# Optimization experiments

Measured on AMD Instinct MI355X. Metric: run time of the kernel, lower is better.

## Reference

```python
import jax, jax.numpy as jnp
import numpy as np
import math

MUL = 128
N_NODES = 10000
N_EDGES = 131072
AVG_NEIGH = 16.0
# (l1 of node irrep, l2 of edge SH, output l3); sorted by output irrep like e3nn Irreps.sort
INSTR = [(0, 0, 0), (1, 1, 0), (0, 1, 1), (1, 0, 1), (1, 2, 1), (0, 2, 2), (1, 1, 2), (1, 3, 2), (0, 3, 3), (1, 2, 3)]
SH_OFF = [0, 1, 4, 9]  # offsets of l-blocks inside edge_attrs (dim 16 = 1+3+5+7)


def _su2_cg(j1, j2, j3):
    f = math.factorial
    C = np.zeros((2 * j1 + 1, 2 * j2 + 1, 2 * j3 + 1))
    for m1 in range(-j1, j1 + 1):
        for m2 in range(-j2, j2 + 1):
            m3 = m1 + m2
            if abs(m3) > j3:
                continue
            pref = (2 * j3 + 1) * f(j3 + j1 - j2) * f(j3 - j1 + j2) * f(j1 + j2 - j3) / f(j1 + j2 + j3 + 1)
            pref *= f(j3 + m3) * f(j3 - m3) * f(j1 - m1) * f(j1 + m1) * f(j2 - m2) * f(j2 + m2)
            s = 0.0
            for k in range(max(0, -(j3 - j2 + m1), -(j3 - j1 - m2)), min(j1 + j2 - j3, j1 - m1, j2 + m2) + 1):
                s += (-1.0) ** k / (f(k) * f(j1 + j2 - j3 - k) * f(j1 - m1 - k) * f(j2 + m2 - k) * f(j3 - j2 + m1 + k) * f(j3 - j1 - m2 + k))
            C[m1 + j1, m2 + j2, m3 + j3] = math.sqrt(pref) * s
    return C


def _q(l):
    # change of basis real->complex spherical harmonics (e3nn convention incl. (-i)^l phase)
    q = np.zeros((2 * l + 1, 2 * l + 1), dtype=np.complex128)
    for m in range(-l, 0):
        q[l + m, l + abs(m)] = 1 / math.sqrt(2)
        q[l + m, l - abs(m)] = -1j / math.sqrt(2)
    q[l, l] = 1.0
    for m in range(1, l + 1):
        q[l + m, l + abs(m)] = (-1) ** m / math.sqrt(2)
        q[l + m, l - abs(m)] = 1j * (-1) ** m / math.sqrt(2)
    return ((-1j) ** l) * q


def _w3j(l1, l2, l3):
    C = _su2_cg(l1, l2, l3).astype(np.complex128)
    Q1, Q2, Q3 = _q(l1), _q(l2), _q(l3)
    for q3 in (np.conj(Q3), Q3):
        D = np.einsum('abc,ai,bj,ck->ijk', C, Q1, Q2, q3)
        if np.abs(D.imag).max() < 1e-9:
            Dr = D.real
            return (Dr / np.linalg.norm(Dr)).astype(np.float32)
    raise ValueError('real wigner-3j construction failed')


W3J = {ins: _w3j(ins[0], ins[1], ins[2]) for ins in set(INSTR)}


def setup_inputs():
    ks = jax.random.split(jax.random.key(0), 15)
    return {
        'node_feats': jax.random.normal(ks[0], (N_NODES, 4 * MUL), jnp.float32),
        'node_attrs': jax.random.normal(ks[1], (N_NODES, 10), jnp.float32),
        'edge_attrs': jax.random.normal(ks[2], (N_EDGES, 16), jnp.float32),
        'edge_feats': jax.random.normal(ks[3], (N_EDGES, 8), jnp.float32),
        'edge_index': jax.random.randint(ks[4], (2, N_EDGES), 0, N_NODES, jnp.int32),
        'W_node_0': jax.random.normal(ks[5], (MUL, MUL), jnp.float32),
        'W_node_1': jax.random.normal(ks[6], (MUL, MUL), jnp.float32),
        'R_W0': jax.random.normal(ks[7], (8, 64), jnp.float32),
        'R_W1': jax.random.normal(ks[8], (64, 64), jnp.float32),
        'R_W2': jax.random.normal(ks[9], (64, 64), jnp.float32),
        'R_W3': jax.random.normal(ks[10], (64, len(INSTR) * MUL), jnp.float32),
        'W_out_0': jax.random.normal(ks[11], (2 * MUL, MUL), jnp.float32),
        'W_out_1': jax.random.normal(ks[12], (3 * MUL, MUL), jnp.float32),
        'W_out_2': jax.random.normal(ks[13], (3 * MUL, MUL), jnp.float32),
        'W_out_3': jax.random.normal(ks[14], (2 * MUL, MUL), jnp.float32),
    }


def reference(node_feats, node_attrs, edge_attrs, edge_feats, edge_index, W_node_0, W_node_1, R_W0, R_W1, R_W2, R_W3, W_out_0, W_out_1, W_out_2, W_out_3):
    sender, receiver = edge_index[0], edge_index[1]
    n = node_feats.shape[0]
    # self-interaction Linear (e3nn: per-irrep matmul, weight / sqrt(fan_in))
    h0 = jnp.einsum('nui,uv->nvi', node_feats[:, :MUL].reshape(n, MUL, 1), W_node_0) / math.sqrt(MUL)
    h1 = jnp.einsum('nui,uv->nvi', node_feats[:, MUL:].reshape(n, MUL, 3), W_node_1) / math.sqrt(MUL)
    # radial MLP [8,64,64,64,1280] with SiLU on hidden layers
    r = edge_feats
    for W in (R_W0, R_W1, R_W2):
        r = jax.nn.silu(r @ (W / math.sqrt(W.shape[0])))
    r = r @ (R_W3 / math.sqrt(R_W3.shape[0]))
    hs = (h0[sender], h1[sender])  # gather sender feats, [E, MUL, 2l1+1]
    outs = {0: [], 1: [], 2: [], 3: []}
    for k, (l1, l2, l3) in enumerate(INSTR):
        w3j = jnp.asarray(W3J[(l1, l2, l3)])
        sh = edge_attrs[:, SH_OFF[l2]:SH_OFF[l2] + 2 * l2 + 1]
        w = r[:, k * MUL:(k + 1) * MUL]
        hw = hs[l1] * w[:, :, None]                                    # radial-weighted sender feats
        c = jnp.einsum('ijk,ej->eik', w3j, sh)                         # [E, 2l1+1, 2l3+1]
        t = jnp.einsum('eik,eui->euk', c, hw) * math.sqrt(2 * l3 + 1)  # 'uvu' path, component-norm path weight
        outs[l3].append(jax.ops.segment_sum(t, receiver, num_segments=n))
    Wout = (W_out_0, W_out_1, W_out_2, W_out_3)
    blocks = []
    for l in range(4):
        cat = jnp.concatenate(outs[l], axis=1)  # simplify(): concat multiplicities per l
        blocks.append(jnp.einsum('nui,uv->nvi', cat, Wout[l]) / (math.sqrt(cat.shape[1]) * AVG_NEIGH))
    return jnp.concatenate(blocks, axis=-1)  # reshape_irreps -> [N, MUL, 16]
```

## Files before the change

kernel.cpp:

```cpp
#include <hip/hip_runtime.h>
#include <math.h>

#define NNODES 10000
#define NEDGES 131072
#define CHUNK 16

#define W3J_OFF 0
#define H_OFF   1280
#define R2_OFF  (1280 + NNODES*512)
#define CSR_W   (R2_OFF + NEDGES*64)
#define CNT_W   CSR_W
#define CUR_W   (CSR_W + NNODES)
#define OFF_W   (CSR_W + 2*NNODES)
#define ELIST_W (CSR_W + 2*NNODES + NNODES + 1)

constexpr int cL1[10]  = {0,1,0,1,1,0,1,1,0,1};
constexpr int cL2[10]  = {0,1,1,0,2,2,1,3,3,2};
constexpr int cN3[10]  = {1,1,3,3,3,5,5,5,7,7};
constexpr int cSHO[10] = {0,1,1,0,4,4,1,9,9,4};
constexpr int cCCO[11] = {0,1,4,7,16,25,30,45,60,67,88};
constexpr int cCATO[10]= {0,128,256,640,1024,1408,2048,2688,3328,4224};

struct cpx { double re, im; };
__device__ inline cpx cmul(cpx a, cpx b){ return {a.re*b.re - a.im*b.im, a.re*b.im + a.im*b.re}; }

__device__ double dfact(int n){ double r = 1.0; for (int i = 2; i <= n; ++i) r *= (double)i; return r; }

__device__ double cgval(int j1,int j2,int j3,int m1,int m2){
  int m3 = m1 + m2;
  if (m3 > j3 || m3 < -j3) return 0.0;
  double pref = (double)(2*j3+1) * dfact(j3+j1-j2)*dfact(j3-j1+j2)*dfact(j1+j2-j3)/dfact(j1+j2+j3+1);
  pref *= dfact(j3+m3)*dfact(j3-m3)*dfact(j1-m1)*dfact(j1+m1)*dfact(j2-m2)*dfact(j2+m2);
  int k0 = 0; if (-(j3-j2+m1) > k0) k0 = -(j3-j2+m1); if (-(j3-j1-m2) > k0) k0 = -(j3-j1-m2);
  int k1 = j1+j2-j3; if (j1-m1 < k1) k1 = j1-m1; if (j2+m2 < k1) k1 = j2+m2;
  double s = 0.0;
  for (int k = k0; k <= k1; ++k){
    double d = dfact(k)*dfact(j1+j2-j3-k)*dfact(j1-m1-k)*dfact(j2+m2-k)*dfact(j3-j2+m1+k)*dfact(j3-j1-m2+k);
    s += ((k & 1) ? -1.0 : 1.0) / d;
  }
  return sqrt(pref) * s;
}

__device__ cpx qval(int l, int a, int col){
  int m = a - l;
  const double is2 = 0.70710678118654752440;
  double re = 0.0, im = 0.0;
  if (m < 0){
    if (col == l - m) re = is2;
    else if (col == l + m) im = -is2;
  } else if (m == 0){
    if (col == l) re = 1.0;
  } else {
    double sgn = (m & 1) ? -1.0 : 1.0;
    if (col == l + m) re = sgn * is2;
    else if (col == l - m) im = sgn * is2;
  }
  double pr, pi;
  switch (l & 3){ case 0: pr=1; pi=0; break; case 1: pr=0; pi=-1; break; case 2: pr=-1; pi=0; break; default: pr=0; pi=1; }
  return { re*pr - im*pi, re*pi + im*pr };
}

__global__ void w3j_kernel(float* ws){
  __shared__ double red[128];
  __shared__ int useConjS;
  __shared__ double normS;
  const int IL[10][3] = {{0,0,0},{1,1,0},{0,1,1},{1,0,1},{1,2,1},{0,2,2},{1,1,2},{1,3,2},{0,3,3},{1,2,3}};
  int k = blockIdx.x;
  int l1 = IL[k][0], l2 = IL[k][1], l3 = IL[k][2];
  int n1 = 2*l1+1, n2 = 2*l2+1, n3 = 2*l3+1;
  int nent = n1*n2*n3;
  int tid = threadIdx.x;
  double dcr=0, dci=0, dpr=0, dpi=0;
  if (tid < nent){
    int i = tid/(n2*n3), j = (tid/n3)%n2, kk = tid%n3;
    for (int a = 0; a < n1; ++a){
      for (int b = 0; b < n2; ++b){
        int m1 = a - l1, m2 = b - l2, m3 = m1 + m2;
        if (m3 < -l3 || m3 > l3) continue;
        int c = m3 + l3;
        double C = cgval(l1,l2,l3,m1,m2);
        if (C == 0.0) continue;
        cpx q1 = qval(l1,a,i), q2 = qval(l2,b,j), q3 = qval(l3,c,kk);
        cpx t = cmul(q1,q2);
        cpx q3c = { q3.re, -q3.im };
        cpx tc = cmul(t, q3c);
        cpx tp = cmul(t, q3);
        dcr += C*tc.re; dci += C*tc.im;
        dpr += C*tp.re; dpi += C*tp.im;
      }
    }
  }
  red[tid] = (tid < nent) ? fabs(dci) : 0.0;
  __syncthreads();
  if (tid == 0){
    double mx = 0.0;
    for (int t = 0; t < 128; ++t) if (red[t] > mx) mx = red[t];
    useConjS = (mx < 1e-9) ? 1 : 0;
  }
  __syncthreads();
  double re = useConjS ? dcr : dpr;
  red[tid] = (tid < nent) ? re*re : 0.0;
  __syncthreads();
  if (tid == 0){
    double s = 0.0;
    for (int t = 0; t < 128; ++t) s += red[t];
    normS = sqrt(s);
  }
  __syncthreads();
  if (tid < nent)
    ws[W3J_OFF + k*128 + tid] = (float)(re / normS * sqrt((double)(2*l3+1)));
}

__launch_bounds__(256, 4)
__global__ void node_kernel(const float* __restrict__ nf, const float* __restrict__ W0,
                            const float* __restrict__ W1, float* __restrict__ ws){
  __shared__ float AtL[128*68];
  float* h = ws + H_OFF;
  int tid = threadIdx.x;
  int n0 = blockIdx.x * 64;
  const float rs = 0.08838834764831845f;
  int mg = (tid & 15) * 4;
  int vg = (tid >> 4) * 8;
  for (int c = 0; c < 4; ++c){
    __syncthreads();
    for (int idx = tid; idx < 8192; idx += 256){
      int m = idx >> 7, u = idx & 127;
      int node = n0 + m;
      float v = 0.f;
      if (node < NNODES)
        v = (c == 0) ? nf[(size_t)node*512 + u] : nf[(size_t)node*512 + 128 + u*3 + (c-1)];
      AtL[u*68 + m] = v;
    }
    __syncthreads();
    const float* W = (c == 0) ? W0 : W1;
    float acc[8][4];
    #pragma unroll
    for (int a = 0; a < 8; ++a){ acc[a][0]=0.f; acc[a][1]=0.f; acc[a][2]=0.f; acc[a][3]=0.f; }
    for (int u = 0; u < 128; ++u){
      float4 am = *(const float4*)&AtL[u*68 + mg];
      const float* wr = W + u*128 + vg;
      float4 b0 = *(const float4*)wr;
      float4 b1 = *(const float4*)(wr + 4);
      float aa[4] = {am.x, am.y, am.z, am.w};
      float bb[8] = {b0.x,b0.y,b0.z,b0.w,b1.x,b1.y,b1.z,b1.w};
      #pragma unroll
      for (int a = 0; a < 8; ++a)
        #pragma unroll
        for (int e = 0; e < 4; ++e)
          acc[a][e] += bb[a]*aa[e];
    }
    #pragma unroll
    for (int e = 0; e < 4; ++e){
      int node = n0 + mg + e;
      if (node < NNODES){
        float4 s0 = {acc[0][e]*rs, acc[1][e]*rs, acc[2][e]*rs, acc[3][e]*rs};
        float4 s1 = {acc[4][e]*rs, acc[5][e]*rs, acc[6][e]*rs, acc[7][e]*rs};
        *(float4*)&h[(size_t)node*512 + c*128 + vg] = s0;
        *(float4*)&h[(size_t)node*512 + c*128 + vg + 4] = s1;
      }
    }
  }
}

template<int KDIM>
__device__ __forceinline__ void mlp_layer(const float* __restrict__ Wg, const float* aL,
                                          float* oL, int tid, float scale){
  int eg = (tid & 15) * 4;
  int jg = (tid >> 4) * 4;
  float acc[4][4];
  #pragma unroll
  for (int a = 0; a < 4; ++a){ acc[a][0]=0.f; acc[a][1]=0.f; acc[a][2]=0.f; acc[a][3]=0.f; }
  #pragma unroll 4
  for (int i = 0; i < KDIM; ++i){
    float4 a4 = *(const float4*)&aL[i*68 + eg];
    float4 b4 = *(const float4*)&Wg[i*64 + jg];
    float aa[4] = {a4.x,a4.y,a4.z,a4.w};
    float bb[4] = {b4.x,b4.y,b4.z,b4.w};
    #pragma unroll
    for (int a = 0; a < 4; ++a)
      #pragma unroll
      for (int e = 0; e < 4; ++e)
        acc[a][e] += bb[a]*aa[e];
  }
  #pragma unroll
  for (int a = 0; a < 4; ++a){
    float4 st;
    float x0 = acc[a][0]*scale; st.x = x0/(1.f + expf(-x0));
    float x1 = acc[a][1]*scale; st.y = x1/(1.f + expf(-x1));
    float x2 = acc[a][2]*scale; st.z = x2/(1.f + expf(-x2));
    float x3 = acc[a][3]*scale; st.w = x3/(1.f + expf(-x3));
    *(float4*)&oL[(jg+a)*68 + eg] = st;
  }
}

__launch_bounds__(256)
__global__ void r2_kernel(const float* __restrict__ ef,
                          const float* __restrict__ RW0, const float* __restrict__ RW1,
                          const float* __restrict__ RW2, float* __restrict__ wsf){
  __shared__ float bufA[64*68];
  __shared__ float bufB[64*68];
  __shared__ float r2T[64*68];
  float* R2 = wsf + R2_OFF;
  int tid = threadIdx.x;
  int eb = blockIdx.x * 64;
  float* efT = r2T;
  for (int idx = tid; idx < 512; idx += 256){
    int e = idx >> 3, i2 = idx & 7;
    efT[i2*68 + e] = ef[(size_t)(eb+e)*8 + i2];
  }
  __syncthreads();
  mlp_layer<8 >(RW0, efT, bufA, tid, 0.35355339059327373f);
  __syncthreads();
  mlp_layer<64>(RW1, bufA, bufB, tid, 0.125f);
  __syncthreads();
  mlp_layer<64>(RW2, bufB, r2T, tid, 0.125f);
  __syncthreads();
  for (int idx = tid; idx < 4096; idx += 256){
    int e = idx >> 6, i = idx & 63;
    R2[((size_t)(eb+e) << 6) + i] = r2T[i*68 + e];
  }
}

__global__ void hist_kernel(const int* __restrict__ ei, int* __restrict__ cnt){
  int e = blockIdx.x*256 + threadIdx.x;
  if (e < NEDGES) atomicAdd(&cnt[ei[NEDGES + e]], 1);
}

__global__ void scan_kernel(const int* __restrict__ cnt, int* __restrict__ off){
  __shared__ int part[256];
  __shared__ int partp[256];
  int t = threadIdx.x;
  const int S = 40;
  int s = 0;
  for (int j = 0; j < S; ++j){ int idx = t*S + j; if (idx < NNODES) s += cnt[idx]; }
  part[t] = s;
  __syncthreads();
  if (t == 0){ int run = 0; for (int i = 0; i < 256; ++i){ partp[i] = run; run += part[i]; } }
  __syncthreads();
  int run = partp[t];
  for (int j = 0; j < S; ++j){
    int idx = t*S + j;
    if (idx <= NNODES){
      off[idx] = run;
      if (idx < NNODES) run += cnt[idx];
    }
  }
}

__global__ void fill_kernel(const int* __restrict__ ei, const int* __restrict__ off,
                            int* __restrict__ cur, int* __restrict__ elist){
  int e = blockIdx.x*256 + threadIdx.x;
  if (e < NEDGES){
    int r = ei[NEDGES + e];
    int p = off[r] + atomicAdd(&cur[r], 1);
    elist[p] = e;
  }
}

__device__ __forceinline__ float cc_compute(int r, const float* w3L, const float* she){
  float v = 0.f;
  #pragma unroll
  for (int in = 0; in < 10; ++in){
    if (r >= cCCO[in] && r < cCCO[in+1]){
      int rr = r - cCCO[in];
      const int N3v = cN3[in];
      const int N2v = 2*cL2[in] + 1;
      int i = rr / N3v;
      int q = rr - i*N3v;
      float s = 0.f;
      for (int j = 0; j < N2v; ++j)
        s += w3L[in*128 + (i*N2v + j)*N3v + q] * she[cSHO[in] + j];
      v = s;
    }
  }
  return v;
}

template<int IN>
__device__ __forceinline__ void tp_one(const float* __restrict__ cce, const float* __restrict__ he,
                                       int u, float wv, float* accm){
  constexpr int N3v = cN3[IN];
  #pragma unroll
  for (int q = 0; q < N3v; ++q){
    float val;
    if constexpr (cL1[IN] == 0)
      val = cce[q] * he[u];
    else
      val = cce[q]*he[128+u] + cce[N3v+q]*he[256+u] + cce[2*N3v+q]*he[384+u];
    accm[q] += wv * val;
  }
}

template<int M>
__device__ __forceinline__ void do_m(const float* __restrict__ RW3, const float* r2L,
                                     const float* ccL, const float* hL,
                                     int tid, int u, int i0, int eN, float* accm){
  float wv[CHUNK];
  #pragma unroll
  for (int e = 0; e < CHUNK; ++e) wv[e] = 0.f;
  const float* rw = RW3 + 256*M + tid;
  #pragma unroll 4
  for (int i = 0; i < 64; ++i){
    float b = rw[(size_t)i*1280];
    const float* rr = &r2L[i*20];
    float4 r0 = *(const float4*)&rr[0];
    float4 r1 = *(const float4*)&rr[4];
    float4 r2v= *(const float4*)&rr[8];
    float4 r3 = *(const float4*)&rr[12];
    wv[0]  += b*r0.x;  wv[1]  += b*r0.y;  wv[2]  += b*r0.z;  wv[3]  += b*r0.w;
    wv[4]  += b*r1.x;  wv[5]  += b*r1.y;  wv[6]  += b*r1.z;  wv[7]  += b*r1.w;
    wv[8]  += b*r2v.x; wv[9]  += b*r2v.y; wv[10] += b*r2v.z; wv[11] += b*r2v.w;
    wv[12] += b*r3.x;  wv[13] += b*r3.y;  wv[14] += b*r3.z;  wv[15] += b*r3.w;
  }
  #pragma unroll
  for (int e = 0; e < CHUNK; ++e) wv[e] *= 0.125f;
  #pragma unroll
  for (int e = 0; e < CHUNK; ++e){
    if (e < eN){
      if (i0 == 0) tp_one<2*M  >(ccL + e*88 + cCCO[2*M  ], hL + (e<<9), u, wv[e], accm);
      else         tp_one<2*M+1>(ccL + e*88 + cCCO[2*M+1], hL + (e<<9), u, wv[e], accm);
    }
  }
}

template<int IN>
__device__ __forceinline__ void st_cat(float* catL, int u, const float* accm){
  constexpr int N3v = cN3[IN];
  float* p = catL + cCATO[IN] + u*N3v;
  #pragma unroll
  for (int q = 0; q < N3v; ++q) p[q] = accm[q];
}

template<int L>
__device__ __forceinline__ void out_g(const float* catL, const float* __restrict__ Wo,
                                      float* redL, float* __restrict__ outp,
                                      int n, int v, int half){
  constexpr int NI = 2*L + 1;
  constexpr int UL = (L==0 || L==3) ? 256 : 384;
  constexpr int GOv = (L==0) ? 0 : (L==1) ? 256 : (L==2) ? 1408 : 3328;
  constexpr int OOv = (L==0) ? 0 : (L==1) ? 1 : (L==2) ? 4 : 9;
  const float scale = (L==0 || L==3) ? 0.00390625f : 0.0031894435433133252f;
  float o[NI];
  #pragma unroll
  for (int i = 0; i < NI; ++i) o[i] = 0.f;
  int ul0 = half * (UL/2);
  for (int ul = ul0; ul < ul0 + UL/2; ++ul){
    float wv = Wo[(size_t)ul*128 + v];
    const float* a = catL + GOv + ul*NI;
    #pragma unroll
    for (int i = 0; i < NI; ++i) o[i] += a[i]*wv;
  }
  if (half == 1){
    #pragma unroll
    for (int i = 0; i < NI; ++i) redL[v*NI + i] = o[i];
  }
  __syncthreads();
  if (half == 0){
    float* op = outp + (size_t)n*2048 + v*16 + OOv;
    #pragma unroll
    for (int i = 0; i < NI; ++i) op[i] = (o[i] + redL[v*NI + i]) * scale;
  }
  __syncthreads();
}

__launch_bounds__(256, 3)
__global__ void gather_kernel(const float* __restrict__ ea, const int* __restrict__ ei,
                              const float* __restrict__ RW3,
                              const float* __restrict__ Wo0, const float* __restrict__ Wo1,
                              const float* __restrict__ Wo2, const float* __restrict__ Wo3,
                              const float* __restrict__ wsf,
                              const int* __restrict__ off, const int* __restrict__ elist,
                              float* __restrict__ outp){
  __shared__ float poolL[CHUNK*512];
  __shared__ float w3L[1280];
  __shared__ float r2L[64*20];
  __shared__ float shL[CHUNK*16];
  __shared__ float ccL[CHUNK*88];
  __shared__ int   idsL[512];
  __shared__ int   idsC[CHUNK];
  __shared__ int   sC[CHUNK];
  const float* h  = wsf + H_OFF;
  const float* R2 = wsf + R2_OFF;
  int nblk = blockIdx.x, tid = threadIdx.x;
  for (int idx = tid; idx < 1280; idx += 256) w3L[idx] = wsf[W3J_OFF + idx];
  int beg = off[nblk], end = off[nblk+1];
  int deg = end - beg;
  int degc = deg < 512 ? deg : 512;
  for (int idx = tid; idx < degc; idx += 256) idsL[idx] = elist[beg + idx];
  __syncthreads();
  for (int p = 0; p < degc; ++p){
    int i1 = 2*tid + (p & 1);
    if (i1 + 1 < degc){
      int a = idsL[i1], b = idsL[i1+1];
      if (b < a){ idsL[i1] = b; idsL[i1+1] = a; }
    }
    __syncthreads();
  }
  int u = tid & 127;
  int i0 = tid >> 7;
  float acc[5][7];
  #pragma unroll
  for (int m = 0; m < 5; ++m)
    #pragma unroll
    for (int q = 0; q < 7; ++q) acc[m][q] = 0.f;

  for (int base = 0; base < deg; base += CHUNK){
    int eN = deg - base; if (eN > CHUNK) eN = CHUNK;
    __syncthreads();
    if (tid < CHUNK){
      int id = 0;
      int k = base + tid;
      if (tid < eN) id = (k < degc) ? idsL[k] : elist[beg + k];
      idsC[tid] = id;
      sC[tid]   = ei[id];
    }
    __syncthreads();
    for (int idx = tid; idx < (eN << 7); idx += 256){
      int e = idx >> 7, j4 = idx & 127;
      *(float4*)&poolL[(e << 9) + j4*4] = *(const float4*)&h[((size_t)sC[e] << 9) + j4*4];
    }
    for (int idx = tid; idx < (eN << 6); idx += 256){
      int e = idx >> 6, i = idx & 63;
      r2L[i*20 + e] = R2[((size_t)idsC[e] << 6) + i];
    }
    for (int idx = tid; idx < (eN << 4); idx += 256){
      int e = idx >> 4, j = idx & 15;
      shL[e*16 + j] = ea[((size_t)idsC[e] << 4) + j];
    }
    __syncthreads();
    for (int idx = tid; idx < eN*88; idx += 256){
      int e = idx / 88, r = idx - e*88;
      ccL[e*88 + r] = cc_compute(r, w3L, shL + e*16);
    }
    __syncthreads();
    do_m<0>(RW3, r2L, ccL, poolL, tid, u, i0, eN, acc[0]);
    do_m<1>(RW3, r2L, ccL, poolL, tid, u, i0, eN, acc[1]);
    do_m<2>(RW3, r2L, ccL, poolL, tid, u, i0, eN, acc[2]);
    do_m<3>(RW3, r2L, ccL, poolL, tid, u, i0, eN, acc[3]);
    do_m<4>(RW3, r2L, ccL, poolL, tid, u, i0, eN, acc[4]);
  }
  __syncthreads();
  float* catL = poolL;
  float* redL = poolL + 5120;
  if (i0 == 0){
    st_cat<0>(catL, u, acc[0]);
    st_cat<2>(catL, u, acc[1]);
    st_cat<4>(catL, u, acc[2]);
    st_cat<6>(catL, u, acc[3]);
    st_cat<8>(catL, u, acc[4]);
  } else {
    st_cat<1>(catL, u, acc[0]);
    st_cat<3>(catL, u, acc[1]);
    st_cat<5>(catL, u, acc[2]);
    st_cat<7>(catL, u, acc[3]);
    st_cat<9>(catL, u, acc[4]);
  }
  __syncthreads();
  out_g<0>(catL, Wo0, redL, outp, nblk, u, i0);
  out_g<1>(catL, Wo1, redL, outp, nblk, u, i0);
  out_g<2>(catL, Wo2, redL, outp, nblk, u, i0);
  out_g<3>(catL, Wo3, redL, outp, nblk, u, i0);
}

extern "C" void kernel_launch(void* const* d_in, const int* in_sizes, int n_in,
                              void* d_out, int out_size, void* d_ws, size_t ws_size,
                              hipStream_t stream){
  const float* nf  = (const float*)d_in[0];
  const float* ea  = (const float*)d_in[2];
  const float* ef  = (const float*)d_in[3];
  const int*   ei  = (const int*)d_in[4];
  const float* W0  = (const float*)d_in[5];
  const float* W1  = (const float*)d_in[6];
  const float* RW0 = (const float*)d_in[7];
  const float* RW1 = (const float*)d_in[8];
  const float* RW2 = (const float*)d_in[9];
  const float* RW3 = (const float*)d_in[10];
  const float* Wo0 = (const float*)d_in[11];
  const float* Wo1 = (const float*)d_in[12];
  const float* Wo2 = (const float*)d_in[13];
  const float* Wo3 = (const float*)d_in[14];
  float* wsf  = (float*)d_ws;
  int*   wsi  = (int*)d_ws;
  float* outp = (float*)d_out;

  hipMemsetAsync(wsi + CNT_W, 0, 2*NNODES*sizeof(int), stream);
  w3j_kernel<<<10, 128, 0, stream>>>(wsf);
  node_kernel<<<157, 256, 0, stream>>>(nf, W0, W1, wsf);
  r2_kernel<<<2048, 256, 0, stream>>>(ef, RW0, RW1, RW2, wsf);
  hist_kernel<<<512, 256, 0, stream>>>(ei, wsi + CNT_W);
  scan_kernel<<<1, 256, 0, stream>>>(wsi + CNT_W, wsi + OFF_W);
  fill_kernel<<<512, 256, 0, stream>>>(ei, wsi + OFF_W, wsi + CUR_W, wsi + ELIST_W);
  gather_kernel<<<NNODES, 256, 0, stream>>>(ea, ei, RW3, Wo0, Wo1, Wo2, Wo3,
                                            wsf, wsi + OFF_W, wsi + ELIST_W, outp);
}
```

Before: 2.159 ms.

## Read sender features directly from global, shrink LDS, rank-sort edge ids

Drops the per-chunk staging of gathered sender features into shared memory. The tensor-product loop now reads h straight from global memory (L2-cached) and always runs a full 16-edge chunk, with padded edges given zero radial weight. The edge-id sort changes from an odd-even transposition sort that synchronises on every pass to a single-pass rank sort. Shared arrays are merged into one overlapping buffer, and accumulators are sized to the real per-path widths, which allows four blocks per CU. In exchange, the same h rows are re-read from global memory once per instruction group, and padded edges do wasted compute.

```diff
diff --git a/kernel.cpp b/kernel.cpp
--- a/kernel.cpp
+++ b/kernel.cpp
@@ -277,24 +277,27 @@
 }
 
 template<int IN>
-__device__ __forceinline__ void tp_one(const float* __restrict__ cce, const float* __restrict__ he,
-                                       int u, float wv, float* accm){
+__device__ __forceinline__ void tp_g(const float* __restrict__ cce, const float* __restrict__ hp,
+                                     float wv, float* accm){
   constexpr int N3v = cN3[IN];
-  #pragma unroll
-  for (int q = 0; q < N3v; ++q){
-    float val;
-    if constexpr (cL1[IN] == 0)
-      val = cce[q] * he[u];
-    else
-      val = cce[q]*he[128+u] + cce[N3v+q]*he[256+u] + cce[2*N3v+q]*he[384+u];
-    accm[q] += wv * val;
+  if constexpr (cL1[IN] == 0){
+    float wh = wv * hp[0];
+    #pragma unroll
+    for (int q = 0; q < N3v; ++q) accm[q] += cce[q] * wh;
+  } else {
+    float wa = wv * hp[128];
+    float wb = wv * hp[256];
+    float wc = wv * hp[384];
+    #pragma unroll
+    for (int q = 0; q < N3v; ++q)
+      accm[q] += cce[q]*wa + cce[N3v+q]*wb + cce[2*N3v+q]*wc;
   }
 }
 
 template<int M>
 __device__ __forceinline__ void do_m(const float* __restrict__ RW3, const float* r2L,
-                                     const float* ccL, const float* hL,
-                                     int tid, int u, int i0, int eN, float* accm){
+                                     const float* ccL, const float* __restrict__ h,
+                                     const int* sC, int tid, int u, int i0, float* accm){
   float wv[CHUNK];
   #pragma unroll
   for (int e = 0; e < CHUNK; ++e) wv[e] = 0.f;
@@ -315,10 +318,21 @@
   #pragma unroll
   for (int e = 0; e < CHUNK; ++e) wv[e] *= 0.125f;
   #pragma unroll
-  for (int e = 0; e < CHUNK; ++e){
-    if (e < eN){
-      if (i0 == 0) tp_one<2*M  >(ccL + e*88 + cCCO[2*M  ], hL + (e<<9), u, wv[e], accm);
-      else         tp_one<2*M+1>(ccL + e*88 + cCCO[2*M+1], hL + (e<<9), u, wv[e], accm);
+  for (int eh = 0; eh < 2; ++eh){
+    if (i0 == 0){
+      #pragma unroll
+      for (int e8 = 0; e8 < 8; ++e8){
+        int e = eh*8 + e8;
+        const float* hp = h + ((size_t)sC[e] << 9) + u;
+        tp_g<2*M>(ccL + e*88 + cCCO[2*M], hp, wv[e], accm);
+      }
+    } else {
+      #pragma unroll
+      for (int e8 = 0; e8 < 8; ++e8){
+        int e = eh*8 + e8;
+        const float* hp = h + ((size_t)sC[e] << 9) + u;
+        tp_g<2*M+1>(ccL + e*88 + cCCO[2*M+1], hp, wv[e], accm);
+      }
     }
   }
 }
@@ -363,7 +377,7 @@
   __syncthreads();
 }
 
-__launch_bounds__(256, 3)
+__launch_bounds__(256, 4)
 __global__ void gather_kernel(const float* __restrict__ ea, const int* __restrict__ ei,
                               const float* __restrict__ RW3,
                               const float* __restrict__ Wo0, const float* __restrict__ Wo1,
@@ -371,14 +385,17 @@
                               const float* __restrict__ wsf,
                               const int* __restrict__ off, const int* __restrict__ elist,
                               float* __restrict__ outp){
-  __shared__ float poolL[CHUNK*512];
-  __shared__ float w3L[1280];
-  __shared__ float r2L[64*20];
-  __shared__ float shL[CHUNK*16];
-  __shared__ float ccL[CHUNK*88];
-  __shared__ int   idsL[512];
-  __shared__ int   idsC[CHUNK];
-  __shared__ int   sC[CHUNK];
+  __shared__ float smemF[6016];
+  int*   idsL = (int*)smemF;
+  int*   idsC = (int*)(smemF + 512);
+  int*   sC   = (int*)(smemF + 528);
+  float* w3L  = smemF + 544;
+  float* r2L  = smemF + 1824;
+  float* shL  = smemF + 3104;
+  float* ccL  = smemF + 3360;
+  float* catL = smemF;
+  float* redL = smemF + 5120;
+
   const float* h  = wsf + H_OFF;
   const float* R2 = wsf + R2_OFF;
   int nblk = blockIdx.x, tid = threadIdx.x;
@@ -388,72 +405,69 @@
   int degc = deg < 512 ? deg : 512;
   for (int idx = tid; idx < degc; idx += 256) idsL[idx] = elist[beg + idx];
   __syncthreads();
-  for (int p = 0; p < degc; ++p){
-    int i1 = 2*tid + (p & 1);
-    if (i1 + 1 < degc){
-      int a = idsL[i1], b = idsL[i1+1];
-      if (b < a){ idsL[i1] = b; idsL[i1+1] = a; }
-    }
-    __syncthreads();
-  }
+  {
+    int v0 = 0, r0 = 0, v1 = 0, r1 = 0;
+    bool a0 = tid < degc, a1 = tid + 256 < degc;
+    if (a0){ v0 = idsL[tid]; int r = 0; for (int j = 0; j < degc; ++j) r += (idsL[j] < v0); r0 = r; }
+    if (a1){ v1 = idsL[tid+256]; int r = 0; for (int j = 0; j < degc; ++j) r += (idsL[j] < v1); r1 = r; }
+    __syncthreads();
+    if (a0) idsL[r0] = v0;
+    if (a1) idsL[r1] = v1;
+  }
+
   int u = tid & 127;
   int i0 = tid >> 7;
-  float acc[5][7];
-  #pragma unroll
-  for (int m = 0; m < 5; ++m)
-    #pragma unroll
-    for (int q = 0; q < 7; ++q) acc[m][q] = 0.f;
+  float acc0[1] = {0.f};
+  float acc1[3] = {0.f,0.f,0.f};
+  float acc2[5] = {0.f,0.f,0.f,0.f,0.f};
+  float acc3[5] = {0.f,0.f,0.f,0.f,0.f};
+  float acc4[7] = {0.f,0.f,0.f,0.f,0.f,0.f,0.f};
 
   for (int base = 0; base < deg; base += CHUNK){
     int eN = deg - base; if (eN > CHUNK) eN = CHUNK;
     __syncthreads();
     if (tid < CHUNK){
-      int id = 0;
       int k = base + tid;
+      int id;
       if (tid < eN) id = (k < degc) ? idsL[k] : elist[beg + k];
+      else          id = (base < degc) ? idsL[base] : elist[beg + base];
       idsC[tid] = id;
       sC[tid]   = ei[id];
     }
     __syncthreads();
-    for (int idx = tid; idx < (eN << 7); idx += 256){
-      int e = idx >> 7, j4 = idx & 127;
-      *(float4*)&poolL[(e << 9) + j4*4] = *(const float4*)&h[((size_t)sC[e] << 9) + j4*4];
-    }
-    for (int idx = tid; idx < (eN << 6); idx += 256){
+    for (int idx = tid; idx < (CHUNK << 6); idx += 256){
       int e = idx >> 6, i = idx & 63;
-      r2L[i*20 + e] = R2[((size_t)idsC[e] << 6) + i];
-    }
-    for (int idx = tid; idx < (eN << 4); idx += 256){
+      r2L[i*20 + e] = (e < eN) ? R2[((size_t)idsC[e] << 6) + i] : 0.f;
+    }
+    for (int idx = tid; idx < (CHUNK << 4); idx += 256){
       int e = idx >> 4, j = idx & 15;
       shL[e*16 + j] = ea[((size_t)idsC[e] << 4) + j];
     }
     __syncthreads();
-    for (int idx = tid; idx < eN*88; idx += 256){
+    for (int idx = tid; idx < CHUNK*88; idx += 256){
       int e = idx / 88, r = idx - e*88;
       ccL[e*88 + r] = cc_compute(r, w3L, shL + e*16);
     }
     __syncthreads();
-    do_m<0>(RW3, r2L, ccL, poolL, tid, u, i0, eN, acc[0]);
-    do_m<1>(RW3, r2L, ccL, poolL, tid, u, i0, eN, acc[1]);
-    do_m<2>(RW3, r2L, ccL, poolL, tid, u, i0, eN, acc[2]);
-    do_m<3>(RW3, r2L, ccL, poolL, tid, u, i0, eN, acc[3]);
-    do_m<4>(RW3, r2L, ccL, poolL, tid, u, i0, eN, acc[4]);
-  }
-  __syncthreads();
-  float* catL = poolL;
-  float* redL = poolL + 5120;
+    do_m<0>(RW3, r2L, ccL, h, sC, tid, u, i0, acc0);
+    do_m<1>(RW3, r2L, ccL, h, sC, tid, u, i0, acc1);
+    do_m<2>(RW3, r2L, ccL, h, sC, tid, u, i0, acc2);
+    do_m<3>(RW3, r2L, ccL, h, sC, tid, u, i0, acc3);
+    do_m<4>(RW3, r2L, ccL, h, sC, tid, u, i0, acc4);
+  }
+  __syncthreads();
   if (i0 == 0){
-    st_cat<0>(catL, u, acc[0]);
-    st_cat<2>(catL, u, acc[1]);
-    st_cat<4>(catL, u, acc[2]);
-    st_cat<6>(catL, u, acc[3]);
-    st_cat<8>(catL, u, acc[4]);
+    st_cat<0>(catL, u, acc0);
+    st_cat<2>(catL, u, acc1);
+    st_cat<4>(catL, u, acc2);
+    st_cat<6>(catL, u, acc3);
+    st_cat<8>(catL, u, acc4);
   } else {
-    st_cat<1>(catL, u, acc[0]);
-    st_cat<3>(catL, u, acc[1]);
-    st_cat<5>(catL, u, acc[2]);
-    st_cat<7>(catL, u, acc[3]);
-    st_cat<9>(catL, u, acc[4]);
+    st_cat<1>(catL, u, acc0);
+    st_cat<3>(catL, u, acc1);
+    st_cat<5>(catL, u, acc2);
+    st_cat<7>(catL, u, acc3);
+    st_cat<9>(catL, u, acc4);
   }
   __syncthreads();
   out_g<0>(catL, Wo0, redL, outp, nblk, u, i0);
```

Measured after the change: 1.893 ms. 1.14x faster.
